# Kernel optimization log

Measured on AMD Instinct MI355X. Metric: run time of the kernel, lower is better.

Reference implementation:

```python
import jax, jax.numpy as jnp
import numpy as np

N = 100000      # nodes
E = 1600000     # nnz of precomputed A^K (avg degree 16)
D = 64          # in_feats
C = 64          # n_classes
LN_EPS = 1e-5


def setup_inputs() -> dict:
    key = jax.random.key(0)
    ks = jax.random.split(key, 8)
    feat = jax.random.normal(ks[0], (N, D), dtype=jnp.float32)
    feat_ori = jax.random.normal(ks[1], (N, D), dtype=jnp.float32)
    row = jax.random.randint(ks[2], (E,), 0, N)
    col = jax.random.randint(ks[3], (E,), 0, N)
    adj_vals = jax.random.uniform(ks[4], (E,), dtype=jnp.float32)
    # Linear params (xavier_uniform weight, zero bias)
    limit = float(np.sqrt(6.0 / (D + C)))
    W = jax.random.uniform(ks[5], (C, D), dtype=jnp.float32, minval=-limit, maxval=limit)
    b = jnp.zeros((C,), dtype=jnp.float32)
    # LayerNorm params
    gamma = jnp.ones((C,), dtype=jnp.float32)
    beta = jnp.zeros((C,), dtype=jnp.float32)
    return {"feat": feat, "feat_ori": feat_ori, "row": row, "col": col,
            "adj_vals": adj_vals, "W": W, "b": b, "gamma": gamma, "beta": beta}


def reference(feat, feat_ori, row, col, adj_vals, W, b, gamma, beta):
    # NOTE: in the source, h = (1-alpha)*feat + alpha*feat_ori is dead code
    # (immediately overwritten by the SpMM of raw feat), so it is omitted.
    # SpMM: h[i] = sum_{e: row[e]=i} adj_vals[e] * feat[col[e]]   -> [N, D]
    msgs = adj_vals[:, None] * feat[col]            # [E, D] gather + scale
    h = jax.ops.segment_sum(msgs, row, num_segments=N)  # [N, D] scatter-add
    # Dense Linear: [N, D] @ [D, C] + [C]
    h = jnp.einsum('nd,cd->nc', h, W) + b
    # LayerNorm over last dim
    mu = jnp.mean(h, axis=-1, keepdims=True)
    var = jnp.mean(jnp.square(h - mu), axis=-1, keepdims=True)
    h = (h - mu) * jax.lax.rsqrt(var + LN_EPS) * gamma + beta
    return h
```

## Files before the change

kernel.cpp:

```cpp
#include <hip/hip_runtime.h>


typedef unsigned int u32;
typedef unsigned short u16;
typedef unsigned long long u64;
#define RFL(x) __builtin_amdgcn_readfirstlane(x)

#define NBLKC 256
#define MAXBK 2048
#define CAP 2048

__device__ __forceinline__ float bf2f(u16 v) {
    return __uint_as_float((u32)v << 16);
}
__device__ __forceinline__ u16 f2bf(float f) {
    u32 b = __float_as_uint(f);
    return (u16)((b + 0x7FFFu + ((b >> 16) & 1u)) >> 16);
}

__global__ __launch_bounds__(256) void k_bhist(const int* __restrict__ row,
                                               u32* __restrict__ hist2d,
                                               int E, int NBK, int CH) {
    __shared__ u32 cnt[MAXBK];
    int tid = threadIdx.x;
    for (int i = tid; i < NBK; i += 256) cnt[i] = 0;
    __syncthreads();
    int e0 = blockIdx.x * CH;
    int e1 = e0 + CH; if (e1 > E) e1 = E;
    int ev = e1 & ~3;
    for (int i = e0 + tid * 4; i < ev; i += 1024) {
        int4 r = *reinterpret_cast<const int4*>(&row[i]);
        atomicAdd(&cnt[(u32)r.x >> 6], 1u);
        atomicAdd(&cnt[(u32)r.y >> 6], 1u);
        atomicAdd(&cnt[(u32)r.z >> 6], 1u);
        atomicAdd(&cnt[(u32)r.w >> 6], 1u);
    }
    { int i = ev + tid; if (i < e1) atomicAdd(&cnt[(u32)row[i] >> 6], 1u); }
    __syncthreads();
    u32* dst = hist2d + (size_t)blockIdx.x * NBK;
    for (int i = tid; i < NBK; i += 256) dst[i] = cnt[i];
}

__device__ __forceinline__ u32 blk_scan256(u32 v, u32* wsum, u32& total) {
    int lane = threadIdx.x & 63, wid = threadIdx.x >> 6;
    u32 incl = v;
#pragma unroll
    for (int o = 1; o < 64; o <<= 1) {
        u32 u = __shfl_up(incl, o);
        if (lane >= o) incl += u;
    }
    if (lane == 63) wsum[wid] = incl;
    __syncthreads();
    u32 woff = 0;
    for (int w = 0; w < wid; ++w) woff += wsum[w];
    total = wsum[0] + wsum[1] + wsum[2] + wsum[3];
    __syncthreads();
    return woff + incl - v;
}

__global__ __launch_bounds__(256) void k_bscan(u32* __restrict__ hist2d,
                                               u32* __restrict__ btot,
                                               int NBLK, int NBK) {
    __shared__ u32 wsum[4];
    int bkt = blockIdx.x;
    u32 carry = 0;
    for (int r = 0; r < NBLK; r += 256) {
        int blk = r + threadIdx.x;
        u32 v = (blk < NBLK) ? hist2d[(size_t)blk * NBK + bkt] : 0;
        u32 tot;
        u32 ex = blk_scan256(v, wsum, tot);
        if (blk < NBLK) hist2d[(size_t)blk * NBK + bkt] = ex + carry;
        carry += tot;
    }
    if (threadIdx.x == 0) btot[bkt] = carry;
}

__global__ __launch_bounds__(256) void k_scanb2(const u32* __restrict__ btot,
                                                u32* __restrict__ bbase,
                                                int NBK, int E) {
    __shared__ u32 wsum[4];
    u32 carry = 0;
    for (int r = 0; r < NBK; r += 256) {
        int i = r + threadIdx.x;
        u32 v = (i < NBK) ? btot[i] : 0;
        u32 tot;
        u32 ex = blk_scan256(v, wsum, tot);
        if (i < NBK) bbase[i] = ex + carry;
        carry += tot;
    }
    if (threadIdx.x == 0) bbase[NBK] = (u32)E;
}

__global__ __launch_bounds__(256) void k_scatgemm(
    const int* __restrict__ row, const int* __restrict__ col,
    const float* __restrict__ vals, const u32* __restrict__ hist2d,
    const u32* __restrict__ bbase, u64* __restrict__ epair1,
    const float* __restrict__ feat, const float* __restrict__ W,
    u16* __restrict__ G, int E, int N, int NBK, int NBLK, int CH)
{
    __shared__ __align__(16) u32 smem[4096];
    int tid = threadIdx.x;
    if ((int)blockIdx.x < NBLK) {
        u32* lbase = smem;
        u32* lcnt  = smem + NBK;
        int blk = blockIdx.x;
        const u32* hrow = hist2d + (size_t)blk * NBK;
        for (int i = tid; i < NBK; i += 256) {
            lbase[i] = bbase[i] + hrow[i];
            lcnt[i] = 0;
        }
        __syncthreads();
        int e0 = blk * CH;
        int e1 = e0 + CH; if (e1 > E) e1 = E;
        int ev = e1 & ~3;
        for (int i = e0 + tid * 4; i < ev; i += 1024) {
            int4 r = *reinterpret_cast<const int4*>(&row[i]);
            int4 c = *reinterpret_cast<const int4*>(&col[i]);
            float4 v = *reinterpret_cast<const float4*>(&vals[i]);
            u32 k0 = (u32)r.x >> 6, k1 = (u32)r.y >> 6;
            u32 k2 = (u32)r.z >> 6, k3 = (u32)r.w >> 6;
            u32 q0 = atomicAdd(&lcnt[k0], 1u);
            u32 q1 = atomicAdd(&lcnt[k1], 1u);
            u32 q2 = atomicAdd(&lcnt[k2], 1u);
            u32 q3 = atomicAdd(&lcnt[k3], 1u);
            epair1[lbase[k0] + q0] = (u64)((u32)c.x | (((u32)r.x & 63u) << 26))
                                   | ((u64)__float_as_uint(v.x) << 32);
            epair1[lbase[k1] + q1] = (u64)((u32)c.y | (((u32)r.y & 63u) << 26))
                                   | ((u64)__float_as_uint(v.y) << 32);
            epair1[lbase[k2] + q2] = (u64)((u32)c.z | (((u32)r.z & 63u) << 26))
                                   | ((u64)__float_as_uint(v.z) << 32);
            epair1[lbase[k3] + q3] = (u64)((u32)c.w | (((u32)r.w & 63u) << 26))
                                   | ((u64)__float_as_uint(v.w) << 32);
        }
        {
            int i = ev + tid;
            if (i < e1) {
                u32 r = (u32)row[i];
                u32 k = r >> 6;
                u32 q = atomicAdd(&lcnt[k], 1u);
                epair1[lbase[k] + q] = (u64)((u32)col[i] | ((r & 63u) << 26))
                                     | ((u64)__float_as_uint(vals[i]) << 32);
            }
        }
    } else {
        float* fs = (float*)smem;
        int lane = tid & 63, wid = tid >> 6;
        int n0 = ((int)blockIdx.x - NBLK) * 64;
        int valid = N - n0; if (valid > 64) valid = 64;
        int elems = valid * 64;
        for (int idx = tid * 4; idx < elems; idx += 1024)
            *reinterpret_cast<float4*>(&fs[idx]) =
                *reinterpret_cast<const float4*>(&feat[(size_t)n0 * 64 + idx]);
        float wr[64];
#pragma unroll
        for (int d4 = 0; d4 < 16; ++d4) {
            float4 w4 = *reinterpret_cast<const float4*>(&W[lane * 64 + d4 * 4]);
            wr[d4 * 4 + 0] = w4.x; wr[d4 * 4 + 1] = w4.y;
            wr[d4 * 4 + 2] = w4.z; wr[d4 * 4 + 3] = w4.w;
        }
        __syncthreads();
        for (int j = 0; j < 16; ++j) {
            int r = wid * 16 + j;
            if (r >= valid) break;
            float o = 0.f;
#pragma unroll
            for (int d4 = 0; d4 < 16; ++d4) {
                float4 h4 = *reinterpret_cast<const float4*>(&fs[r * 64 + d4 * 4]);
                o = fmaf(h4.x, wr[d4 * 4 + 0], o);
                o = fmaf(h4.y, wr[d4 * 4 + 1], o);
                o = fmaf(h4.z, wr[d4 * 4 + 2], o);
                o = fmaf(h4.w, wr[d4 * 4 + 3], o);
            }
            G[(size_t)(n0 + r) * 64 + lane] = f2bf(o);
        }
    }
}

__global__ __launch_bounds__(256) void k_node2(
    const u16* __restrict__ G, const u64* __restrict__ epair1,
    const u32* __restrict__ bbase, const float* __restrict__ bias,
    const float* __restrict__ gamma, const float* __restrict__ beta,
    float* __restrict__ out, int N)
{
    __shared__ u64 sp[CAP];
    __shared__ u32 cnt[64], base[64], cnt2[64];
    int tid = threadIdx.x, lane = tid & 63, wid = tid >> 6;
    int bkt = blockIdx.x;
    if (tid < 64) { cnt[tid] = 0; cnt2[tid] = 0; }
    __syncthreads();
    int s = RFL((int)bbase[bkt]);
    int t = RFL((int)bbase[bkt + 1]);
    int m = t - s;
    bool fits = (m <= CAP);

    const u32* meta1 = (const u32*)epair1;
    for (int i = s + tid; i < t; i += 256)
        atomicAdd(&cnt[meta1[2 * (size_t)i] >> 26], 1u);
    __syncthreads();
    if (tid < 64) {
        u32 v = cnt[tid];
        u32 incl = v;
#pragma unroll
        for (int o = 1; o < 64; o <<= 1) {
            u32 u = __shfl_up(incl, o);
            if (tid >= o) incl += u;
        }
        base[tid] = incl - v;
    }
    __syncthreads();
    if (fits) {
        for (int i = s + tid; i < t; i += 256) {
            u64 p = epair1[i];
            u32 mm = (u32)p;
            u32 r = mm >> 26;
            u32 rank = atomicAdd(&cnt2[r], 1u);
            sp[base[r] + rank] = (p & 0xFFFFFFFF00000000ull) | (u64)(mm & 0x03FFFFFFu);
        }
    }
    __syncthreads();

    int rbase = bkt << 6;
    for (int j = 0; j < 16; ++j) {
        int r = wid * 16 + j;
        int n = rbase + r;
        if (n >= N) break;
        float acc0 = 0.f, acc1 = 0.f;
        if (fits) {
            int e0 = base[r], e1 = base[r] + cnt[r];
            int i = e0;
            for (; i + 8 <= e1; i += 8) {
                u64 p0 = sp[i],     p1 = sp[i + 1];
                u64 p2 = sp[i + 2], p3 = sp[i + 3];
                u64 p4 = sp[i + 4], p5 = sp[i + 5];
                u64 p6 = sp[i + 6], p7 = sp[i + 7];
                u32 c0 = RFL((u32)p0), b0 = RFL((u32)(p0 >> 32));
                u32 c1 = RFL((u32)p1), b1 = RFL((u32)(p1 >> 32));
                u32 c2 = RFL((u32)p2), b2 = RFL((u32)(p2 >> 32));
                u32 c3 = RFL((u32)p3), b3 = RFL((u32)(p3 >> 32));
                u32 c4 = RFL((u32)p4), b4 = RFL((u32)(p4 >> 32));
                u32 c5 = RFL((u32)p5), b5 = RFL((u32)(p5 >> 32));
                u32 c6 = RFL((u32)p6), b6 = RFL((u32)(p6 >> 32));
                u32 c7 = RFL((u32)p7), b7 = RFL((u32)(p7 >> 32));
                float g0 = bf2f(G[((size_t)c0 << 6) | lane]);
                float g1 = bf2f(G[((size_t)c1 << 6) | lane]);
                float g2 = bf2f(G[((size_t)c2 << 6) | lane]);
                float g3 = bf2f(G[((size_t)c3 << 6) | lane]);
                float g4 = bf2f(G[((size_t)c4 << 6) | lane]);
                float g5 = bf2f(G[((size_t)c5 << 6) | lane]);
                float g6 = bf2f(G[((size_t)c6 << 6) | lane]);
                float g7 = bf2f(G[((size_t)c7 << 6) | lane]);
                acc0 = fmaf(__uint_as_float(b0), g0, acc0);
                acc1 = fmaf(__uint_as_float(b1), g1, acc1);
                acc0 = fmaf(__uint_as_float(b2), g2, acc0);
                acc1 = fmaf(__uint_as_float(b3), g3, acc1);
                acc0 = fmaf(__uint_as_float(b4), g4, acc0);
                acc1 = fmaf(__uint_as_float(b5), g5, acc1);
                acc0 = fmaf(__uint_as_float(b6), g6, acc0);
                acc1 = fmaf(__uint_as_float(b7), g7, acc1);
            }
            for (; i < e1; ++i) {
                u64 p = sp[i];
                u32 c = RFL((u32)p), b = RFL((u32)(p >> 32));
                acc0 = fmaf(__uint_as_float(b), bf2f(G[((size_t)c << 6) | lane]), acc0);
            }
        } else {
            for (int i = s; i < t; ++i) {
                u64 p = epair1[i];
                u32 mm = RFL((u32)p);
                if ((int)(mm >> 26) == r) {
                    u32 b = RFL((u32)(p >> 32));
                    acc0 = fmaf(__uint_as_float(b),
                                bf2f(G[((size_t)(mm & 0x03FFFFFFu) << 6) | lane]), acc0);
                }
            }
        }
        float o = acc0 + acc1 + bias[lane];

        float ssum = o;
#pragma unroll
        for (int off = 32; off; off >>= 1) ssum += __shfl_xor(ssum, off);
        float mu = ssum * 0.015625f;
        float dv = o - mu;
        float vs = dv * dv;
#pragma unroll
        for (int off = 32; off; off >>= 1) vs += __shfl_xor(vs, off);
        float inv = rsqrtf(vs * 0.015625f + 1e-5f);
        out[((size_t)n << 6) + lane] = dv * inv * gamma[lane] + beta[lane];
    }
}

extern "C" void kernel_launch(void* const* d_in, const int* in_sizes, int n_in,
                              void* d_out, int out_size, void* d_ws, size_t ws_size,
                              hipStream_t stream) {
    const float* feat  = (const float*)d_in[0];
    const int*   row   = (const int*)d_in[2];
    const int*   col   = (const int*)d_in[3];
    const float* vals  = (const float*)d_in[4];
    const float* W     = (const float*)d_in[5];
    const float* bias  = (const float*)d_in[6];
    const float* gamma = (const float*)d_in[7];
    const float* beta  = (const float*)d_in[8];
    float* out = (float*)d_out;

    const int D = 64;
    int N = in_sizes[0] / D;
    int E = in_sizes[2];

    int NBK  = (N + 63) / 64;
    int NBLK = NBLKC;
    int CH   = (((E + NBLK - 1) / NBLK) + 3) & ~3;
    int NG   = (N + 63) / 64;

    char* ws = (char*)d_ws;
    u16*   G      = (u16*)ws;
    size_t off1   = (((size_t)N * 128) + 255) & ~(size_t)255;
    u64*   epair1 = (u64*)(ws + off1);
    size_t off2   = off1 + (((size_t)E * 8 + 255) & ~(size_t)255);
    u32*   hist2d = (u32*)(ws + off2);
    size_t off3   = off2 + (((size_t)NBLK * NBK * 4 + 255) & ~(size_t)255);
    u32*   btot   = (u32*)(ws + off3);
    u32*   bbase  = btot + NBK;

    k_bhist   <<<NBLK, 256, 0, stream>>>(row, hist2d, E, NBK, CH);
    k_bscan   <<<NBK, 256, 0, stream>>>(hist2d, btot, NBLK, NBK);
    k_scanb2  <<<1, 256, 0, stream>>>(btot, bbase, NBK, E);
    k_scatgemm<<<NBLK + NG, 256, 0, stream>>>(row, col, vals, hist2d, bbase,
                                              epair1, feat, W, G,
                                              E, N, NBK, NBLK, CH);
    k_node2   <<<NBK, 256, 0, stream>>>(G, epair1, bbase, bias, gamma, beta,
                                        out, N);
}
```

Measured before the change: 136.2 us.

## Stage bucketed edges in LDS before scattering, split GEMM into separate kernel

The scatter kernel now uses many small chunks of 3072 edges per block. Each block first counts its edges per bucket, then sorts them locally in shared memory, then writes them to global memory in bucket-contiguous runs, instead of issuing random 8-byte global writes. The fused scatter+GEMM kernel is split into two launches, and the GEMM inner product uses four accumulators to shorten the FMA dependency chain. The trade-offs are an extra pass over row, one more launch, and a much larger hist2d and k_bscan workload because the block count grows to about 521.

```diff
diff --git a/kernel.cpp b/kernel.cpp
--- a/kernel.cpp
+++ b/kernel.cpp
@@ -6,7 +6,7 @@
 typedef unsigned long long u64;
 #define RFL(x) __builtin_amdgcn_readfirstlane(x)
 
-#define NBLKC 256
+#define CHE 3072
 #define MAXBK 2048
 #define CAP 2048
 
@@ -91,88 +91,95 @@
     if (threadIdx.x == 0) bbase[NBK] = (u32)E;
 }
 
-__global__ __launch_bounds__(256) void k_scatgemm(
+__global__ __launch_bounds__(256) void k_scat(
     const int* __restrict__ row, const int* __restrict__ col,
     const float* __restrict__ vals, const u32* __restrict__ hist2d,
     const u32* __restrict__ bbase, u64* __restrict__ epair1,
-    const float* __restrict__ feat, const float* __restrict__ W,
-    u16* __restrict__ G, int E, int N, int NBK, int NBLK, int CH)
+    int E, int NBK, int CH)
 {
-    __shared__ __align__(16) u32 smem[4096];
+    __shared__ u64 sp[CHE];
+    __shared__ u16 sbkt[CHE];
+    __shared__ u32 lbase[MAXBK];
+    __shared__ u32 lcnt[MAXBK];
+    __shared__ u32 locb[MAXBK];
+    __shared__ u32 wsum[4];
     int tid = threadIdx.x;
-    if ((int)blockIdx.x < NBLK) {
-        u32* lbase = smem;
-        u32* lcnt  = smem + NBK;
-        int blk = blockIdx.x;
-        const u32* hrow = hist2d + (size_t)blk * NBK;
-        for (int i = tid; i < NBK; i += 256) {
-            lbase[i] = bbase[i] + hrow[i];
-            lcnt[i] = 0;
-        }
-        __syncthreads();
-        int e0 = blk * CH;
-        int e1 = e0 + CH; if (e1 > E) e1 = E;
-        int ev = e1 & ~3;
-        for (int i = e0 + tid * 4; i < ev; i += 1024) {
-            int4 r = *reinterpret_cast<const int4*>(&row[i]);
-            int4 c = *reinterpret_cast<const int4*>(&col[i]);
-            float4 v = *reinterpret_cast<const float4*>(&vals[i]);
-            u32 k0 = (u32)r.x >> 6, k1 = (u32)r.y >> 6;
-            u32 k2 = (u32)r.z >> 6, k3 = (u32)r.w >> 6;
-            u32 q0 = atomicAdd(&lcnt[k0], 1u);
-            u32 q1 = atomicAdd(&lcnt[k1], 1u);
-            u32 q2 = atomicAdd(&lcnt[k2], 1u);
-            u32 q3 = atomicAdd(&lcnt[k3], 1u);
-            epair1[lbase[k0] + q0] = (u64)((u32)c.x | (((u32)r.x & 63u) << 26))
-                                   | ((u64)__float_as_uint(v.x) << 32);
-            epair1[lbase[k1] + q1] = (u64)((u32)c.y | (((u32)r.y & 63u) << 26))
-                                   | ((u64)__float_as_uint(v.y) << 32);
-            epair1[lbase[k2] + q2] = (u64)((u32)c.z | (((u32)r.z & 63u) << 26))
-                                   | ((u64)__float_as_uint(v.z) << 32);
-            epair1[lbase[k3] + q3] = (u64)((u32)c.w | (((u32)r.w & 63u) << 26))
-                                   | ((u64)__float_as_uint(v.w) << 32);
-        }
-        {
-            int i = ev + tid;
-            if (i < e1) {
-                u32 r = (u32)row[i];
-                u32 k = r >> 6;
-                u32 q = atomicAdd(&lcnt[k], 1u);
-                epair1[lbase[k] + q] = (u64)((u32)col[i] | ((r & 63u) << 26))
-                                     | ((u64)__float_as_uint(vals[i]) << 32);
-            }
-        }
-    } else {
-        float* fs = (float*)smem;
-        int lane = tid & 63, wid = tid >> 6;
-        int n0 = ((int)blockIdx.x - NBLK) * 64;
-        int valid = N - n0; if (valid > 64) valid = 64;
-        int elems = valid * 64;
-        for (int idx = tid * 4; idx < elems; idx += 1024)
-            *reinterpret_cast<float4*>(&fs[idx]) =
-                *reinterpret_cast<const float4*>(&feat[(size_t)n0 * 64 + idx]);
-        float wr[64];
+    int blk = blockIdx.x;
+    const u32* hrow = hist2d + (size_t)blk * NBK;
+    for (int i = tid; i < NBK; i += 256) {
+        lbase[i] = bbase[i] + hrow[i];
+        lcnt[i] = 0;
+    }
+    __syncthreads();
+    int e0 = blk * CH;
+    int e1 = e0 + CH; if (e1 > E) e1 = E;
+    for (int i = e0 + tid; i < e1; i += 256)
+        atomicAdd(&lcnt[(u32)row[i] >> 6], 1u);
+    __syncthreads();
+    {
+        u32 carry = 0;
+        for (int r = 0; r < NBK; r += 256) {
+            int i = r + tid;
+            u32 v = (i < NBK) ? lcnt[i] : 0;
+            u32 tot;
+            u32 ex = blk_scan256(v, wsum, tot);
+            if (i < NBK) locb[i] = ex + carry;
+            carry += tot;
+        }
+    }
+    __syncthreads();
+    for (int i = tid; i < NBK; i += 256) lcnt[i] = 0;
+    __syncthreads();
+    for (int i = e0 + tid; i < e1; i += 256) {
+        u32 r = (u32)row[i];
+        u32 bkt = r >> 6;
+        u32 lrank = atomicAdd(&lcnt[bkt], 1u);
+        u32 slot = locb[bkt] + lrank;
+        sp[slot] = (u64)((u32)col[i] | ((r & 63u) << 26))
+                 | ((u64)__float_as_uint(vals[i]) << 32);
+        sbkt[slot] = (u16)bkt;
+    }
+    __syncthreads();
+    int m = e1 - e0;
+    for (int i = tid; i < m; i += 256) {
+        u32 bkt = sbkt[i];
+        u32 dst = lbase[bkt] + ((u32)i - locb[bkt]);
+        epair1[dst] = sp[i];
+    }
+}
+
+__global__ __launch_bounds__(256) void k_gemm(const float* __restrict__ feat,
+                                              const float* __restrict__ W,
+                                              u16* __restrict__ G, int N) {
+    __shared__ float fs[4096];
+    int lane = threadIdx.x & 63, wid = threadIdx.x >> 6;
+    int n0 = blockIdx.x * 64;
+    int valid = N - n0; if (valid > 64) valid = 64;
+    int elems = valid * 64;
+    for (int idx = threadIdx.x * 4; idx < elems; idx += 1024)
+        *reinterpret_cast<float4*>(&fs[idx]) =
+            *reinterpret_cast<const float4*>(&feat[(size_t)n0 * 64 + idx]);
+    float wr[64];
+#pragma unroll
+    for (int d4 = 0; d4 < 16; ++d4) {
+        float4 w4 = *reinterpret_cast<const float4*>(&W[lane * 64 + d4 * 4]);
+        wr[d4 * 4 + 0] = w4.x; wr[d4 * 4 + 1] = w4.y;
+        wr[d4 * 4 + 2] = w4.z; wr[d4 * 4 + 3] = w4.w;
+    }
+    __syncthreads();
+    for (int j = 0; j < 16; ++j) {
+        int r = wid * 16 + j;
+        if (r >= valid) break;
+        float oa[4] = {0.f, 0.f, 0.f, 0.f};
 #pragma unroll
         for (int d4 = 0; d4 < 16; ++d4) {
-            float4 w4 = *reinterpret_cast<const float4*>(&W[lane * 64 + d4 * 4]);
-            wr[d4 * 4 + 0] = w4.x; wr[d4 * 4 + 1] = w4.y;
-            wr[d4 * 4 + 2] = w4.z; wr[d4 * 4 + 3] = w4.w;
-        }
-        __syncthreads();
-        for (int j = 0; j < 16; ++j) {
-            int r = wid * 16 + j;
-            if (r >= valid) break;
-            float o = 0.f;
-#pragma unroll
-            for (int d4 = 0; d4 < 16; ++d4) {
-                float4 h4 = *reinterpret_cast<const float4*>(&fs[r * 64 + d4 * 4]);
-                o = fmaf(h4.x, wr[d4 * 4 + 0], o);
-                o = fmaf(h4.y, wr[d4 * 4 + 1], o);
-                o = fmaf(h4.z, wr[d4 * 4 + 2], o);
-                o = fmaf(h4.w, wr[d4 * 4 + 3], o);
-            }
-            G[(size_t)(n0 + r) * 64 + lane] = f2bf(o);
-        }
+            float4 h4 = *reinterpret_cast<const float4*>(&fs[r * 64 + d4 * 4]);
+            oa[d4 & 3] = fmaf(h4.x, wr[d4 * 4 + 0],
+                        fmaf(h4.y, wr[d4 * 4 + 1],
+                        fmaf(h4.z, wr[d4 * 4 + 2],
+                        fmaf(h4.w, wr[d4 * 4 + 3], oa[d4 & 3]))));
+        }
+        G[(size_t)(n0 + r) * 64 + lane] = f2bf((oa[0] + oa[1]) + (oa[2] + oa[3]));
     }
 }
 
@@ -307,8 +314,8 @@
     int E = in_sizes[2];
 
     int NBK  = (N + 63) / 64;
-    int NBLK = NBLKC;
-    int CH   = (((E + NBLK - 1) / NBLK) + 3) & ~3;
+    int CH   = CHE;
+    int NBLK = (E + CH - 1) / CH;
     int NG   = (N + 63) / 64;
 
     char* ws = (char*)d_ws;
@@ -321,12 +328,12 @@
     u32*   btot   = (u32*)(ws + off3);
     u32*   bbase  = btot + NBK;
 
-    k_bhist   <<<NBLK, 256, 0, stream>>>(row, hist2d, E, NBK, CH);
-    k_bscan   <<<NBK, 256, 0, stream>>>(hist2d, btot, NBLK, NBK);
-    k_scanb2  <<<1, 256, 0, stream>>>(btot, bbase, NBK, E);
-    k_scatgemm<<<NBLK + NG, 256, 0, stream>>>(row, col, vals, hist2d, bbase,
-                                              epair1, feat, W, G,
-                                              E, N, NBK, NBLK, CH);
-    k_node2   <<<NBK, 256, 0, stream>>>(G, epair1, bbase, bias, gamma, beta,
-                                        out, N);
-}
+    k_bhist <<<NBLK, 256, 0, stream>>>(row, hist2d, E, NBK, CH);
+    k_bscan <<<NBK, 256, 0, stream>>>(hist2d, btot, NBLK, NBK);
+    k_scanb2<<<1, 256, 0, stream>>>(btot, bbase, NBK, E);
+    k_scat  <<<NBLK, 256, 0, stream>>>(row, col, vals, hist2d, bbase,
+                                       epair1, E, NBK, CH);
+    k_gemm  <<<NG, 256, 0, stream>>>(feat, W, G, N);
+    k_node2 <<<NBK, 256, 0, stream>>>(G, epair1, bbase, bias, gamma, beta,
+                                      out, N);
+}
```

Result: slower. 168.7 us (+23.9%).

## Widen scatter/GEMM blocks to 1024 threads and read feat directly per wave

Applied to the files above, without the earlier changes.

Blocks of the fused scatter+GEMM kernel grow from 256 to 1024 threads, so each scatter block covers its edge chunk with four times as many threads. The GEMM part stops staging feat tiles in shared memory and drops its barrier. Each wave now reads its 16 rows straight from global memory as broadcast float4 loads and uses four partial accumulators to shorten the FMA dependency chain. The risk is that launch_bounds(1024,1) limits registers and occupancy, which may cause spills of the 64-float W array. The direct global reads also rely on cache for the broadcast.

```diff
diff --git a/kernel.cpp b/kernel.cpp
--- a/kernel.cpp
+++ b/kernel.cpp
@@ -91,21 +91,21 @@
     if (threadIdx.x == 0) bbase[NBK] = (u32)E;
 }
 
-__global__ __launch_bounds__(256) void k_scatgemm(
+__global__ __launch_bounds__(1024, 1) void k_scatgemm(
     const int* __restrict__ row, const int* __restrict__ col,
     const float* __restrict__ vals, const u32* __restrict__ hist2d,
     const u32* __restrict__ bbase, u64* __restrict__ epair1,
     const float* __restrict__ feat, const float* __restrict__ W,
     u16* __restrict__ G, int E, int N, int NBK, int NBLK, int CH)
 {
-    __shared__ __align__(16) u32 smem[4096];
+    __shared__ u32 smem[2 * MAXBK];
     int tid = threadIdx.x;
     if ((int)blockIdx.x < NBLK) {
         u32* lbase = smem;
         u32* lcnt  = smem + NBK;
         int blk = blockIdx.x;
         const u32* hrow = hist2d + (size_t)blk * NBK;
-        for (int i = tid; i < NBK; i += 256) {
+        for (int i = tid; i < NBK; i += 1024) {
             lbase[i] = bbase[i] + hrow[i];
             lcnt[i] = 0;
         }
@@ -113,7 +113,7 @@
         int e0 = blk * CH;
         int e1 = e0 + CH; if (e1 > E) e1 = E;
         int ev = e1 & ~3;
-        for (int i = e0 + tid * 4; i < ev; i += 1024) {
+        for (int i = e0 + tid * 4; i < ev; i += 4096) {
             int4 r = *reinterpret_cast<const int4*>(&row[i]);
             int4 c = *reinterpret_cast<const int4*>(&col[i]);
             float4 v = *reinterpret_cast<const float4*>(&vals[i]);
@@ -143,14 +143,8 @@
             }
         }
     } else {
-        float* fs = (float*)smem;
         int lane = tid & 63, wid = tid >> 6;
-        int n0 = ((int)blockIdx.x - NBLK) * 64;
-        int valid = N - n0; if (valid > 64) valid = 64;
-        int elems = valid * 64;
-        for (int idx = tid * 4; idx < elems; idx += 1024)
-            *reinterpret_cast<float4*>(&fs[idx]) =
-                *reinterpret_cast<const float4*>(&feat[(size_t)n0 * 64 + idx]);
+        int n0 = ((int)blockIdx.x - NBLK) * 256 + wid * 16;
         float wr[64];
 #pragma unroll
         for (int d4 = 0; d4 < 16; ++d4) {
@@ -158,20 +152,20 @@
             wr[d4 * 4 + 0] = w4.x; wr[d4 * 4 + 1] = w4.y;
             wr[d4 * 4 + 2] = w4.z; wr[d4 * 4 + 3] = w4.w;
         }
-        __syncthreads();
         for (int j = 0; j < 16; ++j) {
-            int r = wid * 16 + j;
-            if (r >= valid) break;
-            float o = 0.f;
+            int r = n0 + j;
+            if (r >= N) break;
+            const float4* fr = reinterpret_cast<const float4*>(&feat[(size_t)r * 64]);
+            float oa[4] = {0.f, 0.f, 0.f, 0.f};
 #pragma unroll
             for (int d4 = 0; d4 < 16; ++d4) {
-                float4 h4 = *reinterpret_cast<const float4*>(&fs[r * 64 + d4 * 4]);
-                o = fmaf(h4.x, wr[d4 * 4 + 0], o);
-                o = fmaf(h4.y, wr[d4 * 4 + 1], o);
-                o = fmaf(h4.z, wr[d4 * 4 + 2], o);
-                o = fmaf(h4.w, wr[d4 * 4 + 3], o);
-            }
-            G[(size_t)(n0 + r) * 64 + lane] = f2bf(o);
+                float4 h4 = fr[d4];
+                oa[d4 & 3] = fmaf(h4.x, wr[d4 * 4 + 0],
+                            fmaf(h4.y, wr[d4 * 4 + 1],
+                            fmaf(h4.z, wr[d4 * 4 + 2],
+                            fmaf(h4.w, wr[d4 * 4 + 3], oa[d4 & 3]))));
+            }
+            G[(size_t)r * 64 + lane] = f2bf((oa[0] + oa[1]) + (oa[2] + oa[3]));
         }
     }
 }
@@ -309,7 +303,7 @@
     int NBK  = (N + 63) / 64;
     int NBLK = NBLKC;
     int CH   = (((E + NBLK - 1) / NBLK) + 3) & ~3;
-    int NG   = (N + 63) / 64;
+    int NG   = (N + 255) / 256;
 
     char* ws = (char*)d_ws;
     u16*   G      = (u16*)ws;
@@ -324,9 +318,9 @@
     k_bhist   <<<NBLK, 256, 0, stream>>>(row, hist2d, E, NBK, CH);
     k_bscan   <<<NBK, 256, 0, stream>>>(hist2d, btot, NBLK, NBK);
     k_scanb2  <<<1, 256, 0, stream>>>(btot, bbase, NBK, E);
-    k_scatgemm<<<NBLK + NG, 256, 0, stream>>>(row, col, vals, hist2d, bbase,
-                                              epair1, feat, W, G,
-                                              E, N, NBK, NBLK, CH);
+    k_scatgemm<<<NBLK + NG, 1024, 0, stream>>>(row, col, vals, hist2d, bbase,
+                                               epair1, feat, W, G,
+                                               E, N, NBK, NBLK, CH);
     k_node2   <<<NBK, 256, 0, stream>>>(G, epair1, bbase, bias, gamma, beta,
                                         out, N);
 }
```

Measured after the change: 369.8 us. 2.72x slower.
